# Optimization experiments

Hardware: AMD Instinct MI355X
Metric: run time of the kernel (lower is better)

Reference implementation:

```python
import jax, jax.numpy as jnp
import numpy as np

D_INPUT, D_MODEL, D_OUTPUT, D_STATE, FACTOR = 100, 256, 100, 64, 2
N2 = D_STATE // 2  # complex conjugate-pair states (S4D)
B_SZ, L_SEQ = 16, 4096


def setup_inputs() -> dict:
    key = jax.random.key(0)
    ks = jax.random.split(key, 12)
    H, N = D_MODEL, N2
    # S4D ('diag-lin', zoh, real_transform='exp') parameters
    log_dt = jax.random.uniform(ks[0], (H,)) * (np.log(0.1) - np.log(0.001)) + np.log(0.001)
    log_A_real = jnp.log(0.5 * jnp.ones((H, N), jnp.float32))
    A_imag = jnp.pi * jnp.broadcast_to(jnp.arange(N, dtype=jnp.float32), (H, N))
    B_re = jnp.ones((H, N), jnp.float32)
    B_im = jnp.zeros((H, N), jnp.float32)
    C_re = jax.random.normal(ks[1], (H, N), jnp.float32)
    C_im = jax.random.normal(ks[2], (H, N), jnp.float32)
    Dskip = jax.random.normal(ks[3], (H,), jnp.float32)
    return {
        'x': jax.random.normal(ks[4], (B_SZ, L_SEQ, D_INPUT), jnp.float32),
        'enc_w': jax.random.normal(ks[5], (D_MODEL, D_INPUT), jnp.float32) / np.sqrt(D_INPUT),
        'enc_b': jnp.zeros((D_MODEL,), jnp.float32),
        'log_dt': log_dt, 'log_A_real': log_A_real, 'A_imag': A_imag,
        'B_re': B_re, 'B_im': B_im, 'C_re': C_re, 'C_im': C_im, 'Dskip': Dskip,
        'ln_g': jnp.ones((D_MODEL,), jnp.float32),
        'ln_b': jnp.zeros((D_MODEL,), jnp.float32),
        'dec1_w': jax.random.normal(ks[6], (D_MODEL * FACTOR, D_MODEL), jnp.float32) / np.sqrt(D_MODEL),
        'dec1_b': jnp.zeros((D_MODEL * FACTOR,), jnp.float32),
        'dec2_w': jax.random.normal(ks[7], (D_OUTPUT, D_MODEL * FACTOR), jnp.float32) / np.sqrt(D_MODEL * FACTOR),
        'dec2_b': jnp.zeros((D_OUTPUT,), jnp.float32),
    }


def s4d_kernel(log_dt, log_A_real, A_imag, B_re, B_im, C_re, C_im, L):
    # diagonal SSM kernel, ZOH discretization: K[h,l] = 2 Re sum_n C'_hn exp(dt_h A_hn)^l
    dt = jnp.exp(log_dt)[:, None]                      # (H,1)
    A = -jnp.exp(log_A_real) + 1j * A_imag             # (H,N)
    C = (B_re + 1j * B_im) * (C_re + 1j * C_im)        # (H,N), B folded into C
    dtA = dt * A                                       # (H,N)
    C = C * (jnp.exp(dtA) - 1.0) / A                   # ZOH correction
    V = jnp.exp(dtA[:, :, None] * jnp.arange(L))       # (H,N,L) Vandermonde
    return 2.0 * jnp.einsum('hn,hnl->hl', C, V).real   # (H,L)


def reference(x, enc_w, enc_b, log_dt, log_A_real, A_imag, B_re, B_im, C_re, C_im,
              Dskip, ln_g, ln_b, dec1_w, dec1_b, dec2_w, dec2_b):
    B, L, _ = x.shape
    u = (x @ enc_w.T + enc_b).transpose(0, 2, 1)       # (B,H,L)
    # FFTConv (single layer), dropout = identity (eval)
    k = s4d_kernel(log_dt, log_A_real, A_imag, B_re, B_im, C_re, C_im, L)
    n = 2 * L
    y = jnp.fft.irfft(jnp.fft.rfft(u, n=n) * jnp.fft.rfft(k, n=n)[None], n=n)[..., :L]
    y = y + u * Dskip[None, :, None]
    y = jax.nn.gelu(y, approximate=False)
    h = y + u                                          # residual
    # LayerNorm over channel dim
    t = h.transpose(0, 2, 1)                           # (B,L,H)
    mu = t.mean(-1, keepdims=True)
    var = jnp.mean((t - mu) ** 2, axis=-1, keepdims=True)
    t = (t - mu) / jnp.sqrt(var + 1e-5) * ln_g + ln_b
    # decoder MLP
    out = jax.nn.gelu(t @ dec1_w.T + dec1_b, approximate=False) @ dec2_w.T + dec2_b
    return out
```

## Files before the change

kernel.cpp:

```cpp
#include <hip/hip_runtime.h>
#include <hip/hip_bf16.h>

#define BB    16
#define LL    4096
#define DIN   100
#define HD    256
#define NN    32
#define DHID  512
#define DOUT  100
#define MROWS (BB*LL)
#define CH    64
#define CC    64
#define NCH   (BB*CC)

#define OFF_WRE    0
#define OFF_WIM    8192
#define OFF_KRE    16384
#define OFF_KIM    24576
#define OFF_WCHR   32768
#define OFF_WCHI   40960
#define OFF_ENCB   49152
#define OFF_DSK    49408
#define OFF_LNG    49664
#define OFF_LNB    49920
#define OFF_B1     50176
#define OFF_B2     50688
#define OFF_WENCB  50816
#define OFF_W1B    67200
#define OFF_W2B    132736
#define OFF_WFL    165504
#define OFF_BY     1230464
#define OFF_VST    2279040
#define OFF_UH     2803328
#define OFF_S      11191936
#define OFF_YH     19580544
#define OFF_TB     OFF_S
#define OFF_G0     OFF_UH
#define OFF_G1     OFF_YH

typedef __bf16 bf16x8 __attribute__((ext_vector_type(8)));
typedef float  f32x4  __attribute__((ext_vector_type(4)));

static __device__ __forceinline__ int probe_bf16(const void* lng) {
    return ((const unsigned int*)lng)[0] != 0x3f800000u;
}
static __device__ __forceinline__ float ldin(const void* p, long i, int isbf) {
    return isbf ? __bfloat162float(((const __hip_bfloat16*)p)[i]) : ((const float*)p)[i];
}
static __device__ __forceinline__ void stout(void* p, long i, float v, int isbf) {
    if (isbf) ((__hip_bfloat16*)p)[i] = __float2bfloat16(v);
    else      ((float*)p)[i] = v;
}
static __device__ __forceinline__ unsigned short f2bf(float v) {
    union { float f; unsigned u; } c; c.f = v;
    unsigned r = c.u + 0x7fffu + ((c.u >> 16) & 1u);
    return (unsigned short)(r >> 16);
}
static __device__ __forceinline__ float bf2f(unsigned short v) {
    union { unsigned u; float f; } c; c.u = ((unsigned)v) << 16; return c.f;
}
static __device__ __forceinline__ float gelu_f(float x) {
    float z  = fabsf(x) * 0.70710678118654752f;
    float tt = __builtin_amdgcn_rcpf(fmaf(0.3275911f, z, 1.0f));
    float p  = tt * fmaf(tt, fmaf(tt, fmaf(tt, fmaf(tt, 1.061405429f, -1.453152027f),
                          1.421413741f), -0.284496736f), 0.254829592f);
    float er = 1.0f - p * __expf(-z * z);
    return 0.5f * x * (1.0f + copysignf(er, x));
}
static __device__ __forceinline__ void gl2lds16(const unsigned short* g, unsigned short* l) {
    __builtin_amdgcn_global_load_lds(
        (const __attribute__((address_space(1))) unsigned int*)g,
        (__attribute__((address_space(3))) unsigned int*)l, 16, 0, 0);
}

__global__ __launch_bounds__(256) void k_prep(
    const void* encw, const void* encb, const void* logdt, const void* loga,
    const void* aim, const void* bre, const void* bim, const void* cre,
    const void* cim, const void* dsk, const void* lng, const void* lnb,
    const void* w1, const void* b1, const void* w2, const void* b2, float* ws)
{
    const int isbf = probe_bf16(lng);
    unsigned short* WEB = (unsigned short*)(ws + OFF_WENCB);
    unsigned short* W1B = (unsigned short*)(ws + OFF_W1B);
    unsigned short* W2B = (unsigned short*)(ws + OFF_W2B);
    const int total = 8192 + 256*4 + 512 + 128 + 32768 + 131072 + 65536;
    for (int idx = blockIdx.x * blockDim.x + threadIdx.x; idx < total;
         idx += gridDim.x * blockDim.x) {
        int i = idx;
        if (i < 8192) {
            int h = i >> 5;
            float dt  = expf(ldin(logdt, h, isbf));
            float Are = -expf(ldin(loga, i, isbf));
            float Aim = ldin(aim, i, isbf);
            float er  = expf(dt * Are);
            float sv, cv; sincosf(dt * Aim, &sv, &cv);
            float wre = er * cv, wim = er * sv;
            float Bre = ldin(bre, i, isbf), Bim = ldin(bim, i, isbf);
            float Cre = ldin(cre, i, isbf), Cim = ldin(cim, i, isbf);
            float C0re = Bre*Cre - Bim*Cim;
            float C0im = Bre*Cim + Bim*Cre;
            float inv = 1.0f / (Are*Are + Aim*Aim);
            float nre = wre - 1.0f, nim = wim;
            float Zre = (nre*Are + nim*Aim) * inv;
            float Zim = (nim*Are - nre*Aim) * inv;
            float kre = 2.0f * (C0re*Zre - C0im*Zim);
            float kim = -2.0f * (C0re*Zim + C0im*Zre);
            ws[OFF_WRE + i] = wre;  ws[OFF_WIM + i] = wim;
            ws[OFF_KRE + i] = kre;  ws[OFF_KIM + i] = kim;
            int n = i & 31; (void)n;
            float* Wf = ws + OFF_WFL + (long)h * 4160 + 2*(i & 31);
            float pr = 1.0f, pi = 0.0f;
            for (int d = 0; d <= 64; ++d) {
                Wf[d*64]     = pr;
                Wf[d*64 + 1] = pi;
                float tr = pr*wre - pi*wim;
                pi = pr*wim + pi*wre; pr = tr;
            }
            ws[OFF_WCHR + i] = Wf[64*64];
            ws[OFF_WCHI + i] = Wf[64*64 + 1];
        } else if ((i -= 8192) < 256) {
            ws[OFF_ENCB + i] = ldin(encb, i, isbf);
        } else if ((i -= 256) < 256) {
            ws[OFF_DSK + i] = ldin(dsk, i, isbf);
        } else if ((i -= 256) < 256) {
            ws[OFF_LNG + i] = ldin(lng, i, isbf);
        } else if ((i -= 256) < 256) {
            ws[OFF_LNB + i] = ldin(lnb, i, isbf);
        } else if ((i -= 256) < 512) {
            ws[OFF_B1 + i] = ldin(b1, i, isbf);
        } else if ((i -= 512) < 128) {
            ws[OFF_B2 + i] = (i < 100) ? ldin(b2, i, isbf) : 0.0f;
        } else if ((i -= 128) < 32768) {
            int h = i >> 7, k = i & 127;
            WEB[i] = (k < 100) ? f2bf(ldin(encw, (long)h*100 + k, isbf)) : (unsigned short)0;
        } else if ((i -= 32768) < 131072) {
            W1B[i] = f2bf(ldin(w1, i, isbf));
        } else if ((i -= 131072) < 65536) {
            int j = i >> 9, k = i & 511;
            W2B[i] = (j < 100) ? f2bf(ldin(w2, (long)j*512 + k, isbf)) : (unsigned short)0;
        }
    }
}

__global__ __launch_bounds__(256) void k_tker(float* ws)
{
    __shared__ float Wp[65*65];
    __shared__ float kr[32], ki[32], Ks[64];
    int h = blockIdx.x;
    int t = threadIdx.x;
    for (int idx = t; idx < 4160; idx += 256) {
        int d = idx >> 6, c = idx & 63;
        Wp[d*65 + c] = ws[OFF_WFL + (long)h*4160 + idx];
    }
    if (t < 32) kr[t] = ws[OFF_KRE + h*32 + t];
    else if (t < 64) ki[t-32] = ws[OFF_KIM + h*32 + (t-32)];
    __syncthreads();
    if (t < 64) {
        float s = 0.0f;
        #pragma unroll
        for (int n = 0; n < 32; ++n)
            s += kr[n]*Wp[t*65 + 2*n] + ki[n]*Wp[t*65 + 2*n + 1];
        Ks[t] = s;
    }
    __syncthreads();
    unsigned short* BY = (unsigned short*)(ws + OFF_BY) + (long)h*8192;
    for (int idx = t; idx < 8192; idx += 256) {
        int j = idx >> 7, k = idx & 127;
        float v;
        if (k < 64) {
            v = (k <= j) ? Ks[j - k] : 0.0f;
        } else {
            int c = k - 64, n = c >> 1;
            float pr = Wp[(j+1)*65 + 2*n], pi = Wp[(j+1)*65 + 2*n + 1];
            v = ((c & 1) == 0) ? (kr[n]*pr + ki[n]*pi) : (ki[n]*pr - kr[n]*pi);
        }
        BY[idx] = f2bf(v);
    }
    unsigned short* Vst = (unsigned short*)(ws + OFF_VST) + (long)h*4096;
    for (int idx = t; idx < 4096; idx += 256) {
        int comp = idx >> 6, i = idx & 63;
        Vst[idx] = f2bf(Wp[(63 - i)*65 + comp]);
    }
}

__global__ __launch_bounds__(256) void k_encm(const void* x, const void* lng, float* ws)
{
    const int isbf = probe_bf16(lng);
    __shared__ unsigned short SM[18432];
    unsigned short (*As)[72] = (unsigned short(*)[72])SM;
    unsigned short (*Bs)[72] = (unsigned short(*)[72])(SM + 9216);
    unsigned short* Cs = SM;
    const unsigned short* WEB = (const unsigned short*)(ws + OFF_WENCB);
    int bid = blockIdx.x;
    int rt = bid >> 1, ct = bid & 1;
    long row0 = (long)rt * 128;
    int c0 = ct * 128;
    int t = threadIdx.x;
    int lane = t & 63, wv = t >> 6;
    int wm = (wv & 1) * 64, wn = (wv >> 1) * 64;
    int quad = lane >> 4, mr = lane & 15;
    f32x4 acc[4][4] = {};
    for (int kc = 0; kc < 2; ++kc) {
        int k0 = kc * 64;
        for (int idx = t; idx < 128*64; idx += 256) {
            int r = idx >> 6, k = idx & 63;
            int kg = k0 + k;
            float v = (kg < 100) ? ldin(x, (row0 + r)*100 + kg, isbf) : 0.0f;
            As[r][k] = f2bf(v);
        }
        for (int idx = t; idx < 128*32; idx += 256) {
            int r = idx >> 5, kk = idx & 31;
            ((unsigned int*)&Bs[r][0])[kk] =
                ((const unsigned int*)WEB)[((c0 + r) * 128 + k0) / 2 + kk];
        }
        __syncthreads();
        #pragma unroll
        for (int ks = 0; ks < 64; ks += 32) {
            bf16x8 af[4], bfr[4];
            #pragma unroll
            for (int i = 0; i < 4; ++i)
                af[i] = *(const bf16x8*)&As[wm + i*16 + mr][ks + quad*8];
            #pragma unroll
            for (int j = 0; j < 4; ++j)
                bfr[j] = *(const bf16x8*)&Bs[wn + j*16 + mr][ks + quad*8];
            #pragma unroll
            for (int i = 0; i < 4; ++i)
                #pragma unroll
                for (int j = 0; j < 4; ++j)
                    acc[i][j] = __builtin_amdgcn_mfma_f32_16x16x32_bf16(af[i], bfr[j], acc[i][j], 0, 0, 0);
        }
        __syncthreads();
    }
    const float* eb = ws + OFF_ENCB;
    #pragma unroll
    for (int j = 0; j < 4; ++j) {
        int hloc = wn + j*16 + mr;
        float bb = eb[c0 + hloc];
        #pragma unroll
        for (int i = 0; i < 4; ++i) {
            int l0 = wm + i*16 + quad*4;
            unsigned short pk[4];
            #pragma unroll
            for (int reg = 0; reg < 4; ++reg)
                pk[reg] = f2bf(acc[i][j][reg] + bb);
            *(uint2*)&Cs[hloc*136 + l0] = *(uint2*)pk;
        }
    }
    __syncthreads();
    unsigned short* Uh = (unsigned short*)(ws + OFF_UH);
    #pragma unroll
    for (int it = 0; it < 8; ++it) {
        int idx = t + it*256;
        int hh = idx >> 4, f = idx & 15;
        *(float4*)&Uh[(long)(c0 + hh)*65536 + row0 + f*8] = *(const float4*)&Cs[hh*136 + f*8];
    }
}

__global__ __launch_bounds__(256) void k_state(float* ws)
{
    __shared__ unsigned short As[128][72];
    __shared__ unsigned short Bs[64][72];
    const unsigned short* Uh  = (const unsigned short*)(ws + OFF_UH);
    const unsigned short* Vst = (const unsigned short*)(ws + OFF_VST);
    int bid = blockIdx.x;
    int h = bid >> 3, ct = bid & 7;
    int c0r = ct * 128;
    int t = threadIdx.x;
    int lane = t & 63, wv = t >> 6;
    int wm = (wv & 1) * 64, wn = (wv >> 1) * 32;
    int quad = lane >> 4, mr = lane & 15;
    const unsigned short* Ubase = Uh + (long)h * 65536;
    #pragma unroll
    for (int it = 0; it < 4; ++it) {
        int idx = t + it*256;
        int r = idx >> 3, f = idx & 7;
        *(float4*)&As[r][f*8] = *(const float4*)&Ubase[(long)(c0r + r)*64 + f*8];
    }
    #pragma unroll
    for (int it = 0; it < 2; ++it) {
        int idx = t + it*256;
        int r = idx >> 3, f = idx & 7;
        *(float4*)&Bs[r][f*8] = *(const float4*)&Vst[(long)h*4096 + r*64 + f*8];
    }
    __syncthreads();
    f32x4 acc[4][2] = {};
    #pragma unroll
    for (int ks = 0; ks < 64; ks += 32) {
        bf16x8 af[4], bfr[2];
        #pragma unroll
        for (int i = 0; i < 4; ++i)
            af[i] = *(const bf16x8*)&As[wm + i*16 + mr][ks + quad*8];
        #pragma unroll
        for (int jn = 0; jn < 2; ++jn)
            bfr[jn] = *(const bf16x8*)&Bs[wn + jn*16 + mr][ks + quad*8];
        #pragma unroll
        for (int i = 0; i < 4; ++i)
            #pragma unroll
            for (int jn = 0; jn < 2; ++jn)
                acc[i][jn] = __builtin_amdgcn_mfma_f32_16x16x32_bf16(af[i], bfr[jn], acc[i][jn], 0, 0, 0);
    }
    __syncthreads();
    unsigned short* Cs = &As[0][0];
    #pragma unroll
    for (int jn = 0; jn < 2; ++jn) {
        int c = wn + jn*16 + mr;
        #pragma unroll
        for (int i = 0; i < 4; ++i)
            #pragma unroll
            for (int reg = 0; reg < 4; ++reg)
                Cs[(wm + i*16 + quad*4 + reg)*72 + c] = f2bf(acc[i][jn][reg]);
    }
    __syncthreads();
    unsigned short* S = (unsigned short*)(ws + OFF_S);
    #pragma unroll
    for (int it = 0; it < 4; ++it) {
        int idx = t + it*256;
        int r = idx >> 3, f = idx & 7;
        *(float4*)&S[(long)(c0r + r)*16384 + h*64 + f*8] = *(const float4*)&Cs[r*72 + f*8];
    }
}

__global__ __launch_bounds__(256) void k_chunk(float* ws)
{
    int tid = blockIdx.x * 256 + threadIdx.x;
    int b = tid >> 13;
    int h = (tid >> 5) & 255;
    int n = tid & 31;
    int i = h * NN + n;
    float wr = ws[OFF_WCHR + i], wi = ws[OFF_WCHI + i];
    unsigned int* Su = (unsigned int*)(ws + OFF_S);
    long a0 = (long)(b * CC) * 8192 + h * 32 + n;
    float rr = 0.0f, ri = 0.0f;
    unsigned int vnext = Su[a0];
    for (int c = 0; c < CC; ++c) {
        long a = a0 + (long)c * 8192;
        unsigned int v = vnext;
        if (c + 1 < CC) vnext = Su[a + 8192];
        float Sr = bf2f((unsigned short)(v & 0xFFFFu));
        float Si = bf2f((unsigned short)(v >> 16));
        Su[a] = (unsigned int)f2bf(rr) | ((unsigned int)f2bf(ri) << 16);
        float nr = fmaf(wr, rr, fmaf(-wi, ri, Sr));
        float ni = fmaf(wr, ri, fmaf(wi, rr, Si));
        rr = nr; ri = ni;
    }
}

__global__ __launch_bounds__(256) void k_y(float* ws)
{
    __shared__ unsigned short As[128][136];
    __shared__ unsigned short Bs[64][136];
    const unsigned short* Uh = (const unsigned short*)(ws + OFF_UH);
    const unsigned short* S  = (const unsigned short*)(ws + OFF_S);
    const unsigned short* BY = (const unsigned short*)(ws + OFF_BY);
    int bid = blockIdx.x;
    int h = bid >> 3, ct = bid & 7;
    int c0r = ct * 128;
    int t = threadIdx.x;
    int lane = t & 63, wv = t >> 6;
    int wm = (wv & 1) * 64, wn = (wv >> 1) * 32;
    int quad = lane >> 4, mr = lane & 15;
    #pragma unroll
    for (int it = 0; it < 8; ++it) {
        int idx = t + it*256;
        int r = idx >> 4, f = idx & 15;
        const unsigned short* src = (f < 8)
            ? &Uh[(long)h*65536 + (long)(c0r + r)*64 + f*8]
            : &S[(long)(c0r + r)*16384 + h*64 + (f-8)*8];
        *(float4*)&As[r][f*8] = *(const float4*)src;
    }
    #pragma unroll
    for (int it = 0; it < 4; ++it) {
        int idx = t + it*256;
        int r = idx >> 4, f = idx & 15;
        *(float4*)&Bs[r][f*8] = *(const float4*)&BY[(long)h*8192 + r*128 + f*8];
    }
    __syncthreads();
    f32x4 acc[4][2] = {};
    #pragma unroll
    for (int ks = 0; ks < 128; ks += 32) {
        bf16x8 af[4], bfr[2];
        #pragma unroll
        for (int i = 0; i < 4; ++i)
            af[i] = *(const bf16x8*)&As[wm + i*16 + mr][ks + quad*8];
        #pragma unroll
        for (int jn = 0; jn < 2; ++jn)
            bfr[jn] = *(const bf16x8*)&Bs[wn + jn*16 + mr][ks + quad*8];
        #pragma unroll
        for (int i = 0; i < 4; ++i)
            #pragma unroll
            for (int jn = 0; jn < 2; ++jn)
                acc[i][jn] = __builtin_amdgcn_mfma_f32_16x16x32_bf16(af[i], bfr[jn], acc[i][jn], 0, 0, 0);
    }
    __syncthreads();
    unsigned short* Cs = &As[0][0];
    #pragma unroll
    for (int jn = 0; jn < 2; ++jn) {
        int c = wn + jn*16 + mr;
        #pragma unroll
        for (int i = 0; i < 4; ++i)
            #pragma unroll
            for (int reg = 0; reg < 4; ++reg)
                Cs[(wm + i*16 + quad*4 + reg)*136 + c] = f2bf(acc[i][jn][reg]);
    }
    __syncthreads();
    unsigned short* Yh = (unsigned short*)(ws + OFF_YH);
    #pragma unroll
    for (int it = 0; it < 4; ++it) {
        int idx = t + it*256;
        int r = idx >> 3, f = idx & 7;
        *(float4*)&Yh[(long)h*65536 + (long)(c0r + r)*64 + f*8] = *(const float4*)&Cs[r*136 + f*8];
    }
}

__global__ __launch_bounds__(1024) void k_ln2(float* ws)
{
    __shared__ unsigned short Vs[64][258];
    __shared__ float parts[64][17], partq[64][17];
    __shared__ float Ms[64], Rs[64];
    __shared__ float Dls[256], Gls[256], Bls[256];
    int chunk = blockIdx.x;
    int t = threadIdx.x;
    if (t < 256) { Dls[t] = ws[OFF_DSK + t]; Gls[t] = ws[OFF_LNG + t]; Bls[t] = ws[OFF_LNB + t]; }
    __syncthreads();
    const unsigned short* Uh = (const unsigned short*)(ws + OFF_UH);
    const unsigned short* Yh = (const unsigned short*)(ws + OFF_YH);
    int j = t & 63, hg = t >> 6;
    float ps = 0.0f, pq = 0.0f;
    #pragma unroll 4
    for (int k = 0; k < 16; ++k) {
        int h = hg*16 + k;
        long base = (long)h*65536 + chunk*64;
        float u = bf2f(Uh[base + j]);
        float y = bf2f(Yh[base + j]);
        float v = gelu_f(fmaf(Dls[h], u, y)) + u;
        Vs[j][h] = f2bf(v);
        ps += v; pq += v*v;
    }
    parts[j][hg] = ps; partq[j][hg] = pq;
    __syncthreads();
    if (t < 64) {
        float s = 0.0f, q = 0.0f;
        #pragma unroll
        for (int g = 0; g < 16; ++g) { s += parts[t][g]; q += partq[t][g]; }
        float mean = s * (1.0f/256.0f);
        float var  = q * (1.0f/256.0f) - mean*mean;
        Ms[t] = mean; Rs[t] = rsqrtf(var + 1e-5f);
    }
    __syncthreads();
    unsigned short* Tb = (unsigned short*)(ws + OFF_TB);
    int h2 = t & 255, jg = t >> 8;
    #pragma unroll 4
    for (int jj = 0; jj < 16; ++jj) {
        int j2 = jg*16 + jj;
        float v = bf2f(Vs[j2][h2]);
        Tb[((long)chunk*64 + j2)*256 + h2] = f2bf((v - Ms[j2]) * Rs[j2] * Gls[h2] + Bls[h2]);
    }
}

__global__ __launch_bounds__(256) void k_dec1m(float* ws)
{
    __shared__ unsigned short SM[18432];
    unsigned short* As = SM;
    unsigned short* Bs = SM + 8192;
    unsigned short* Cs = SM;
    const unsigned short* Tb  = (const unsigned short*)(ws + OFF_TB);
    const unsigned short* W1B = (const unsigned short*)(ws + OFF_W1B);
    int bid = blockIdx.x;
    int rt = bid >> 2, ct = bid & 3;
    long row0 = (long)rt * 128;
    int c0 = ct * 128;
    int t = threadIdx.x;
    int lane = t & 63, wv = t >> 6;
    int wm = (wv & 1) * 64, wn = (wv >> 1) * 64;
    int quad = lane >> 4, mr = lane & 15;
    int swz = lane & 7;
    int sr = t >> 3;
    int sdst = (t & 7) * 8;
    int ssrc = ((t & 7) ^ (sr & 7)) * 8;
    f32x4 acc[4][4] = {};
    for (int kc = 0; kc < 4; ++kc) {
        int k0 = kc * 64;
        #pragma unroll
        for (int it = 0; it < 4; ++it) {
            int r = sr + it * 32;
            gl2lds16(&Tb[(row0 + r) * 256 + k0 + ssrc], &As[r * 64 + sdst]);
        }
        #pragma unroll
        for (int it = 0; it < 4; ++it) {
            int r = sr + it * 32;
            gl2lds16(&W1B[(long)(c0 + r) * 256 + k0 + ssrc], &Bs[r * 64 + sdst]);
        }
        __syncthreads();
        #pragma unroll
        for (int ks = 0; ks < 64; ks += 32) {
            int co = (((ks >> 3) | quad) ^ swz) * 8;
            bf16x8 af[4], bfr[4];
            #pragma unroll
            for (int i = 0; i < 4; ++i)
                af[i] = *(const bf16x8*)&As[(wm + i*16 + mr)*64 + co];
            #pragma unroll
            for (int j = 0; j < 4; ++j)
                bfr[j] = *(const bf16x8*)&Bs[(wn + j*16 + mr)*64 + co];
            #pragma unroll
            for (int i = 0; i < 4; ++i)
                #pragma unroll
                for (int j = 0; j < 4; ++j)
                    acc[i][j] = __builtin_amdgcn_mfma_f32_16x16x32_bf16(af[i], bfr[j], acc[i][j], 0, 0, 0);
        }
        __syncthreads();
    }
    const float* b1 = ws + OFF_B1;
    #pragma unroll
    for (int j = 0; j < 4; ++j) {
        int cloc = wn + j*16 + mr;
        float bb = b1[c0 + cloc];
        #pragma unroll
        for (int i = 0; i < 4; ++i)
            #pragma unroll
            for (int reg = 0; reg < 4; ++reg)
                Cs[(wm + i*16 + quad*4 + reg)*136 + cloc] = f2bf(gelu_f(acc[i][j][reg] + bb));
    }
    __syncthreads();
    unsigned short* G = (unsigned short*)(ws + ((ct < 2) ? OFF_G0 : OFF_G1));
    int cl0 = (ct < 2) ? c0 : (c0 - 256);
    #pragma unroll
    for (int it = 0; it < 8; ++it) {
        int idx = t + it*256;
        int r = idx >> 4, f = idx & 15;
        *(float4*)&G[(row0 + r)*256 + cl0 + f*8] = *(const float4*)&Cs[r*136 + f*8];
    }
}

__global__ __launch_bounds__(256) void k_dec2m(float* ws, void* out, const void* lng)
{
    const int isbf = probe_bf16(lng);
    __shared__ unsigned short SM[18432];
    unsigned short* As = SM;
    unsigned short* Bs = SM + 8192;
    unsigned short* Cs = SM;
    const unsigned short* G0  = (const unsigned short*)(ws + OFF_G0);
    const unsigned short* G1  = (const unsigned short*)(ws + OFF_G1);
    const unsigned short* W2B = (const unsigned short*)(ws + OFF_W2B);
    long row0 = (long)blockIdx.x * 128;
    int t = threadIdx.x;
    int lane = t & 63, wv = t >> 6;
    int wm = (wv & 1) * 64, wn = (wv >> 1) * 64;
    int quad = lane >> 4, mr = lane & 15;
    int swz = lane & 7;
    int sr = t >> 3;
    int sdst = (t & 7) * 8;
    int ssrc = ((t & 7) ^ (sr & 7)) * 8;
    f32x4 acc[4][4] = {};
    for (int kc = 0; kc < 8; ++kc) {
        int k0 = kc * 64;
        const unsigned short* Gsrc = (kc < 4) ? G0 : G1;
        int kl = (kc < 4) ? k0 : (k0 - 256);
        #pragma unroll
        for (int it = 0; it < 4; ++it) {
            int r = sr + it * 32;
            gl2lds16(&Gsrc[(row0 + r) * 256 + kl + ssrc], &As[r * 64 + sdst]);
        }
        #pragma unroll
        for (int it = 0; it < 4; ++it) {
            int r = sr + it * 32;
            gl2lds16(&W2B[(long)r * 512 + k0 + ssrc], &Bs[r * 64 + sdst]);
        }
        __syncthreads();
        #pragma unroll
        for (int ks = 0; ks < 64; ks += 32) {
            int co = (((ks >> 3) | quad) ^ swz) * 8;
            bf16x8 af[4], bfr[4];
            #pragma unroll
            for (int i = 0; i < 4; ++i)
                af[i] = *(const bf16x8*)&As[(wm + i*16 + mr)*64 + co];
            #pragma unroll
            for (int j = 0; j < 4; ++j)
                bfr[j] = *(const bf16x8*)&Bs[(wn + j*16 + mr)*64 + co];
            #pragma unroll
            for (int i = 0; i < 4; ++i)
                #pragma unroll
                for (int j = 0; j < 4; ++j)
                    acc[i][j] = __builtin_amdgcn_mfma_f32_16x16x32_bf16(af[i], bfr[j], acc[i][j], 0, 0, 0);
        }
        __syncthreads();
    }
    const float* b2 = ws + OFF_B2;
    if (isbf) {
        #pragma unroll
        for (int j = 0; j < 4; ++j) {
            int cloc = wn + j*16 + mr;
            float bb = b2[cloc];
            #pragma unroll
            for (int i = 0; i < 4; ++i)
                #pragma unroll
                for (int reg = 0; reg < 4; ++reg)
                    Cs[(wm + i*16 + quad*4 + reg)*136 + cloc] = f2bf(acc[i][j][reg] + bb);
        }
        __syncthreads();
        for (int idx = t; idx < 128*25; idx += 256) {
            int r = idx / 25, f = idx % 25;
            uint2* dst = (uint2*)((char*)out + (row0 + r)*200);
            dst[f] = *(const uint2*)&Cs[r*136 + f*4];
        }
    } else {
        #pragma unroll
        for (int j = 0; j < 4; ++j) {
            int col = wn + j*16 + mr;
            if (col < 100) {
                float bb = b2[col];
                #pragma unroll
                for (int i = 0; i < 4; ++i)
                    #pragma unroll
                    for (int reg = 0; reg < 4; ++reg) {
                        long row = row0 + wm + i*16 + quad*4 + reg;
                        ((float*)out)[row * 100 + col] = acc[i][j][reg] + bb;
                    }
            }
        }
    }
}

extern "C" void kernel_launch(void* const* d_in, const int* in_sizes, int n_in,
                              void* d_out, int out_size, void* d_ws, size_t ws_size,
                              hipStream_t stream)
{
    float* ws = (float*)d_ws;
    k_prep<<<512, 256, 0, stream>>>(d_in[1], d_in[2], d_in[3], d_in[4], d_in[5],
                                    d_in[6], d_in[7], d_in[8], d_in[9], d_in[10],
                                    d_in[11], d_in[12], d_in[13], d_in[14],
                                    d_in[15], d_in[16], ws);
    k_tker<<<256, 256, 0, stream>>>(ws);
    k_encm<<<1024, 256, 0, stream>>>(d_in[0], d_in[11], ws);
    k_state<<<2048, 256, 0, stream>>>(ws);
    k_chunk<<<512, 256, 0, stream>>>(ws);
    k_y<<<2048, 256, 0, stream>>>(ws);
    k_ln2<<<NCH, 1024, 0, stream>>>(ws);
    k_dec1m<<<2048, 256, 0, stream>>>(ws);
    k_dec2m<<<512, 256, 0, stream>>>(ws, d_out, d_in[11]);
}
```

Before: 308.0 us.

## Pre-convert input to padded bf16 and double-buffer LDS in the three GEMMs

Adds a kernel that converts x to a padded bf16 row layout (128 columns), so the encoder GEMM can use async global-to-LDS loads with a swizzled layout instead of scalar converting loads. The encoder, dec1 and dec2 GEMMs now double-buffer LDS and issue the next K-chunk's loads before computing the current one, aiming to overlap memory traffic with MFMA work. The cost is an extra kernel launch and round trip through workspace for x, plus twice the LDS per block, which may lower occupancy.

After: 273.0 us. -11.3%, faster.

```diff
diff --git a/kernel.cpp b/kernel.cpp
--- a/kernel.cpp
+++ b/kernel.cpp
@@ -37,6 +37,7 @@
 #define OFF_TB     OFF_S
 #define OFF_G0     OFF_UH
 #define OFF_G1     OFF_YH
+#define OFF_XB     OFF_YH
 
 typedef __bf16 bf16x8 __attribute__((ext_vector_type(8)));
 typedef float  f32x4  __attribute__((ext_vector_type(4)));
@@ -46,10 +47,6 @@
 }
 static __device__ __forceinline__ float ldin(const void* p, long i, int isbf) {
     return isbf ? __bfloat162float(((const __hip_bfloat16*)p)[i]) : ((const float*)p)[i];
-}
-static __device__ __forceinline__ void stout(void* p, long i, float v, int isbf) {
-    if (isbf) ((__hip_bfloat16*)p)[i] = __float2bfloat16(v);
-    else      ((float*)p)[i] = v;
 }
 static __device__ __forceinline__ unsigned short f2bf(float v) {
     union { float f; unsigned u; } c; c.f = v;
@@ -107,7 +104,6 @@
             float kim = -2.0f * (C0re*Zim + C0im*Zre);
             ws[OFF_WRE + i] = wre;  ws[OFF_WIM + i] = wim;
             ws[OFF_KRE + i] = kre;  ws[OFF_KIM + i] = kim;
-            int n = i & 31; (void)n;
             float* Wf = ws + OFF_WFL + (long)h * 4160 + 2*(i & 31);
             float pr = 1.0f, pi = 0.0f;
             for (int d = 0; d <= 64; ++d) {
@@ -142,6 +138,47 @@
     }
 }
 
+__global__ __launch_bounds__(256) void k_xcvt(const void* x, const void* lng, float* ws)
+{
+    const int isbf = probe_bf16(lng);
+    unsigned short* Xb = (unsigned short*)(ws + OFF_XB);
+    const int total = 65536 * 16;
+    for (int s = blockIdx.x * 256 + threadIdx.x; s < total; s += 1024 * 256) {
+        int row = s >> 4, slot = s & 15;
+        int k0 = slot * 8;
+        unsigned short pk[8];
+        if (!isbf) {
+            const float* xr = (const float*)x + (long)row * 100;
+            if (slot < 12) {
+                float4 a = *(const float4*)(xr + k0);
+                float4 b = *(const float4*)(xr + k0 + 4);
+                pk[0]=f2bf(a.x); pk[1]=f2bf(a.y); pk[2]=f2bf(a.z); pk[3]=f2bf(a.w);
+                pk[4]=f2bf(b.x); pk[5]=f2bf(b.y); pk[6]=f2bf(b.z); pk[7]=f2bf(b.w);
+            } else if (slot == 12) {
+                float4 a = *(const float4*)(xr + 96);
+                pk[0]=f2bf(a.x); pk[1]=f2bf(a.y); pk[2]=f2bf(a.z); pk[3]=f2bf(a.w);
+                pk[4]=0; pk[5]=0; pk[6]=0; pk[7]=0;
+            } else {
+                #pragma unroll
+                for (int j = 0; j < 8; ++j) pk[j] = 0;
+            }
+        } else {
+            const unsigned short* xr = (const unsigned short*)x + (long)row * 100;
+            if (slot < 12) {
+                *(uint2*)&pk[0] = *(const uint2*)(xr + k0);
+                *(uint2*)&pk[4] = *(const uint2*)(xr + k0 + 4);
+            } else if (slot == 12) {
+                *(uint2*)&pk[0] = *(const uint2*)(xr + 96);
+                pk[4]=0; pk[5]=0; pk[6]=0; pk[7]=0;
+            } else {
+                #pragma unroll
+                for (int j = 0; j < 8; ++j) pk[j] = 0;
+            }
+        }
+        *(float4*)&Xb[(long)row * 128 + k0] = *(const float4*)pk;
+    }
+}
+
 __global__ __launch_bounds__(256) void k_tker(float* ws)
 {
     __shared__ float Wp[65*65];
@@ -183,13 +220,11 @@
     }
 }
 
-__global__ __launch_bounds__(256) void k_encm(const void* x, const void* lng, float* ws)
-{
-    const int isbf = probe_bf16(lng);
-    __shared__ unsigned short SM[18432];
-    unsigned short (*As)[72] = (unsigned short(*)[72])SM;
-    unsigned short (*Bs)[72] = (unsigned short(*)[72])(SM + 9216);
+__global__ __launch_bounds__(256) void k_encm(float* ws)
+{
+    __shared__ unsigned short SM[32768];
     unsigned short* Cs = SM;
+    const unsigned short* Xb  = (const unsigned short*)(ws + OFF_XB);
     const unsigned short* WEB = (const unsigned short*)(ws + OFF_WENCB);
     int bid = blockIdx.x;
     int rt = bid >> 1, ct = bid & 1;
@@ -199,30 +234,38 @@
     int lane = t & 63, wv = t >> 6;
     int wm = (wv & 1) * 64, wn = (wv >> 1) * 64;
     int quad = lane >> 4, mr = lane & 15;
+    int swz = lane & 7;
+    int sr = t >> 3, sdst = (t & 7) * 8, ssrc = ((t & 7) ^ (sr & 7)) * 8;
     f32x4 acc[4][4] = {};
+    #pragma unroll
+    for (int it = 0; it < 4; ++it) {
+        int r = sr + it * 32;
+        gl2lds16(&Xb[(row0 + r) * 128 + ssrc], &SM[r * 64 + sdst]);
+        gl2lds16(&WEB[(long)(c0 + r) * 128 + ssrc], &SM[8192 + r * 64 + sdst]);
+    }
+    __syncthreads();
+    #pragma unroll
     for (int kc = 0; kc < 2; ++kc) {
-        int k0 = kc * 64;
-        for (int idx = t; idx < 128*64; idx += 256) {
-            int r = idx >> 6, k = idx & 63;
-            int kg = k0 + k;
-            float v = (kg < 100) ? ldin(x, (row0 + r)*100 + kg, isbf) : 0.0f;
-            As[r][k] = f2bf(v);
-        }
-        for (int idx = t; idx < 128*32; idx += 256) {
-            int r = idx >> 5, kk = idx & 31;
-            ((unsigned int*)&Bs[r][0])[kk] =
-                ((const unsigned int*)WEB)[((c0 + r) * 128 + k0) / 2 + kk];
-        }
-        __syncthreads();
+        const unsigned short* As = &SM[(kc & 1) * 16384];
+        const unsigned short* Bs = As + 8192;
+        if (kc == 0) {
+            #pragma unroll
+            for (int it = 0; it < 4; ++it) {
+                int r = sr + it * 32;
+                gl2lds16(&Xb[(row0 + r) * 128 + 64 + ssrc], &SM[16384 + r * 64 + sdst]);
+                gl2lds16(&WEB[(long)(c0 + r) * 128 + 64 + ssrc], &SM[24576 + r * 64 + sdst]);
+            }
+        }
         #pragma unroll
         for (int ks = 0; ks < 64; ks += 32) {
+            int co = (((ks >> 3) | quad) ^ swz) * 8;
             bf16x8 af[4], bfr[4];
             #pragma unroll
             for (int i = 0; i < 4; ++i)
-                af[i] = *(const bf16x8*)&As[wm + i*16 + mr][ks + quad*8];
+                af[i] = *(const bf16x8*)&As[(wm + i*16 + mr)*64 + co];
             #pragma unroll
             for (int j = 0; j < 4; ++j)
-                bfr[j] = *(const bf16x8*)&Bs[wn + j*16 + mr][ks + quad*8];
+                bfr[j] = *(const bf16x8*)&Bs[(wn + j*16 + mr)*64 + co];
             #pragma unroll
             for (int i = 0; i < 4; ++i)
                 #pragma unroll
@@ -459,9 +502,7 @@
 
 __global__ __launch_bounds__(256) void k_dec1m(float* ws)
 {
-    __shared__ unsigned short SM[18432];
-    unsigned short* As = SM;
-    unsigned short* Bs = SM + 8192;
+    __shared__ unsigned short SM[32768];
     unsigned short* Cs = SM;
     const unsigned short* Tb  = (const unsigned short*)(ws + OFF_TB);
     const unsigned short* W1B = (const unsigned short*)(ws + OFF_W1B);
@@ -474,23 +515,29 @@
     int wm = (wv & 1) * 64, wn = (wv >> 1) * 64;
     int quad = lane >> 4, mr = lane & 15;
     int swz = lane & 7;
-    int sr = t >> 3;
-    int sdst = (t & 7) * 8;
-    int ssrc = ((t & 7) ^ (sr & 7)) * 8;
+    int sr = t >> 3, sdst = (t & 7) * 8, ssrc = ((t & 7) ^ (sr & 7)) * 8;
     f32x4 acc[4][4] = {};
+    #pragma unroll
+    for (int it = 0; it < 4; ++it) {
+        int r = sr + it * 32;
+        gl2lds16(&Tb[(row0 + r) * 256 + ssrc], &SM[r * 64 + sdst]);
+        gl2lds16(&W1B[(long)(c0 + r) * 256 + ssrc], &SM[8192 + r * 64 + sdst]);
+    }
+    __syncthreads();
+    #pragma unroll
     for (int kc = 0; kc < 4; ++kc) {
-        int k0 = kc * 64;
-        #pragma unroll
-        for (int it = 0; it < 4; ++it) {
-            int r = sr + it * 32;
-            gl2lds16(&Tb[(row0 + r) * 256 + k0 + ssrc], &As[r * 64 + sdst]);
-        }
-        #pragma unroll
-        for (int it = 0; it < 4; ++it) {
-            int r = sr + it * 32;
-            gl2lds16(&W1B[(long)(c0 + r) * 256 + k0 + ssrc], &Bs[r * 64 + sdst]);
-        }
-        __syncthreads();
+        const unsigned short* As = &SM[(kc & 1) * 16384];
+        const unsigned short* Bs = As + 8192;
+        if (kc < 3) {
+            int k0 = (kc + 1) * 64;
+            unsigned short* Dst = &SM[((kc + 1) & 1) * 16384];
+            #pragma unroll
+            for (int it = 0; it < 4; ++it) {
+                int r = sr + it * 32;
+                gl2lds16(&Tb[(row0 + r) * 256 + k0 + ssrc], &Dst[r * 64 + sdst]);
+                gl2lds16(&W1B[(long)(c0 + r) * 256 + k0 + ssrc], &Dst[8192 + r * 64 + sdst]);
+            }
+        }
         #pragma unroll
         for (int ks = 0; ks < 64; ks += 32) {
             int co = (((ks >> 3) | quad) ^ swz) * 8;
@@ -534,9 +581,7 @@
 __global__ __launch_bounds__(256) void k_dec2m(float* ws, void* out, const void* lng)
 {
     const int isbf = probe_bf16(lng);
-    __shared__ unsigned short SM[18432];
-    unsigned short* As = SM;
-    unsigned short* Bs = SM + 8192;
+    __shared__ unsigned short SM[32768];
     unsigned short* Cs = SM;
     const unsigned short* G0  = (const unsigned short*)(ws + OFF_G0);
     const unsigned short* G1  = (const unsigned short*)(ws + OFF_G1);
@@ -547,25 +592,32 @@
     int wm = (wv & 1) * 64, wn = (wv >> 1) * 64;
     int quad = lane >> 4, mr = lane & 15;
     int swz = lane & 7;
-    int sr = t >> 3;
-    int sdst = (t & 7) * 8;
-    int ssrc = ((t & 7) ^ (sr & 7)) * 8;
+    int sr = t >> 3, sdst = (t & 7) * 8, ssrc = ((t & 7) ^ (sr & 7)) * 8;
     f32x4 acc[4][4] = {};
+    #pragma unroll
+    for (int it = 0; it < 4; ++it) {
+        int r = sr + it * 32;
+        gl2lds16(&G0[(row0 + r) * 256 + ssrc], &SM[r * 64 + sdst]);
+        gl2lds16(&W2B[(long)r * 512 + ssrc], &SM[8192 + r * 64 + sdst]);
+    }
+    __syncthreads();
+    #pragma unroll
     for (int kc = 0; kc < 8; ++kc) {
-        int k0 = kc * 64;
-        const unsigned short* Gsrc = (kc < 4) ? G0 : G1;
-        int kl = (kc < 4) ? k0 : (k0 - 256);
-        #pragma unroll
-        for (int it = 0; it < 4; ++it) {
-            int r = sr + it * 32;
-            gl2lds16(&Gsrc[(row0 + r) * 256 + kl + ssrc], &As[r * 64 + sdst]);
-        }
-        #pragma unroll
-        for (int it = 0; it < 4; ++it) {
-            int r = sr + it * 32;
-            gl2lds16(&W2B[(long)r * 512 + k0 + ssrc], &Bs[r * 64 + sdst]);
-        }
-        __syncthreads();
+        const unsigned short* As = &SM[(kc & 1) * 16384];
+        const unsigned short* Bs = As + 8192;
+        if (kc < 7) {
+            int s = kc + 1;
+            const unsigned short* Gsrc = (s < 4) ? G0 : G1;
+            int kl = (s & 3) * 64;
+            int k0 = s * 64;
+            unsigned short* Dst = &SM[(s & 1) * 16384];
+            #pragma unroll
+            for (int it = 0; it < 4; ++it) {
+                int r = sr + it * 32;
+                gl2lds16(&Gsrc[(row0 + r) * 256 + kl + ssrc], &Dst[r * 64 + sdst]);
+                gl2lds16(&W2B[(long)r * 512 + k0 + ssrc], &Dst[8192 + r * 64 + sdst]);
+            }
+        }
         #pragma unroll
         for (int ks = 0; ks < 64; ks += 32) {
             int co = (((ks >> 3) | quad) ^ swz) * 8;
@@ -629,8 +681,9 @@
                                     d_in[6], d_in[7], d_in[8], d_in[9], d_in[10],
                                     d_in[11], d_in[12], d_in[13], d_in[14],
                                     d_in[15], d_in[16], ws);
+    k_xcvt<<<1024, 256, 0, stream>>>(d_in[0], d_in[11], ws);
     k_tker<<<256, 256, 0, stream>>>(ws);
-    k_encm<<<1024, 256, 0, stream>>>(d_in[0], d_in[11], ws);
+    k_encm<<<1024, 256, 0, stream>>>(ws);
     k_state<<<2048, 256, 0, stream>>>(ws);
     k_chunk<<<512, 256, 0, stream>>>(ws);
     k_y<<<2048, 256, 0, stream>>>(ws);
```
